# Kernel tuning notes

Hardware: AMD Instinct MI355X
Metric: run time of the kernel (lower is better)

The kernel has to match this reference:

```python
import jax, jax.numpy as jnp
import numpy as np

D_MODEL = 1024
N_HEADS = 16
HEAD_DIM = D_MODEL // N_HEADS
EPS = 1e-6


def setup_inputs() -> dict:
    key = jax.random.key(0)
    ks = jax.random.split(key, 5)
    b, s = 2, 2048
    x = jax.random.normal(ks[0], (b, s, D_MODEL), dtype=jnp.float32)
    scale = 1.0 / np.sqrt(D_MODEL)
    Wq = jax.random.normal(ks[1], (D_MODEL, D_MODEL), dtype=jnp.float32) * scale
    Wk = jax.random.normal(ks[2], (D_MODEL, D_MODEL), dtype=jnp.float32) * scale
    Wv = jax.random.normal(ks[3], (D_MODEL, D_MODEL), dtype=jnp.float32) * scale
    Wo = jax.random.normal(ks[4], (D_MODEL, D_MODEL), dtype=jnp.float32) * scale
    return {"x": x, "Wq": Wq, "Wk": Wk, "Wv": Wv, "Wo": Wo}


def _feature_map(t):
    return jax.nn.relu(t) + EPS


def reference(x, Wq, Wk, Wv, Wo):
    b, s, _ = x.shape
    # nn.Linear applies x @ W.T
    q = (x @ Wq.T).reshape(b, s, N_HEADS, HEAD_DIM)
    k = (x @ Wk.T).reshape(b, s, N_HEADS, HEAD_DIM)
    v = (x @ Wv.T).reshape(b, s, N_HEADS, HEAD_DIM)
    q = _feature_map(q).transpose(0, 2, 1, 3)  # bhsd
    k = _feature_map(k).transpose(0, 2, 1, 3)  # bhsd
    v = v.transpose(0, 2, 1, 3)                # bhsm
    # cumulative KV outer products: (b,h,s,d,m)
    kv = jnp.einsum('bhsd,bhsm->bhsdm', k, v)
    kv_cum = jnp.cumsum(kv, axis=2)
    out = jnp.einsum('bhsd,bhsdm->bhsm', q, kv_cum)
    k_cum = jnp.cumsum(k, axis=2)
    z = 1.0 / (jnp.einsum('bhsd,bhsd->bhs', q, k_cum) + EPS)
    out = out * z[..., None]
    out = out.transpose(0, 2, 1, 3).reshape(b, s, D_MODEL)
    return out @ Wo.T
```

## Files before the change

### kernel.cpp

```cpp
#include <hip/hip_runtime.h>

#define EPSF 1e-6f

typedef short bf16x8_t __attribute__((ext_vector_type(8)));
typedef float f32x4_t __attribute__((ext_vector_type(4)));

__device__ __forceinline__ ushort f2bf(float f) {
  union { float f; uint32_t u; } c; c.f = f;
  return (ushort)((c.u + 0x7FFFu + ((c.u >> 16) & 1u)) >> 16);
}
__device__ __forceinline__ float bf2f(ushort u) {
  union { uint32_t u; float f; } c; c.u = ((uint32_t)u) << 16;
  return c.f;
}

#define SWB(row, kbyte) (((row) << 7) + ((kbyte) ^ (((row) & 7) << 4)))

__global__ __launch_bounds__(256) void cvt5_kernel(
    const float4* __restrict__ x, const float4* __restrict__ wq,
    const float4* __restrict__ wk, const float4* __restrict__ wv,
    const float4* __restrict__ wo,
    ushort4* __restrict__ xb, ushort4* __restrict__ wqb,
    ushort4* __restrict__ wkb, ushort4* __restrict__ wvb,
    ushort4* __restrict__ wob)
{
  const int i = blockIdx.x * 256 + threadIdx.x;
  const float4* src; ushort4* dst; int off;
  if (i < (1 << 20)) { src = x; dst = xb; off = i; }
  else {
    const int j = i - (1 << 20);
    const int r = j >> 18;
    off = j & ((1 << 18) - 1);
    src = (r == 0) ? wq : (r == 1) ? wk : (r == 2) ? wv : wo;
    dst = (r == 0) ? wqb : (r == 1) ? wkb : (r == 2) ? wvb : wob;
  }
  const float4 v = src[off];
  ushort4 o;
  o.x = f2bf(v.x); o.y = f2bf(v.y); o.z = f2bf(v.z); o.w = f2bf(v.w);
  dst[off] = o;
}

template<int OUT_BF16, int ATOMIC>
__device__ __forceinline__ void gemm_bt_mfma(
    const ushort* __restrict__ A, const ushort* __restrict__ B,
    void* __restrict__ C, const int K,
    const int kbeg, const int kend,
    const int N, const int row0, const int col0, const bool relu)
{
  __shared__ __align__(16) uint As[2048];
  __shared__ __align__(16) uint Bs[2048];
  const int tid = threadIdx.x;
  const int lane = tid & 63;
  const int wv = tid >> 6;
  const int wr = (wv >> 1) * 64;
  const int wc = (wv & 1) * 64;

  f32x4_t acc[4][4];
#pragma unroll
  for (int m = 0; m < 4; ++m)
#pragma unroll
    for (int n = 0; n < 4; ++n) acc[m][n] = (f32x4_t){0.f, 0.f, 0.f, 0.f};

  const int fr = lane & 15;
  const int kh = (lane >> 4) * 8;

  const int chunk0 = wv * 64 + lane;
  const int chunk1 = chunk0 + 256;
  const int row_0 = chunk0 >> 2, kp0 = (chunk0 & 3) << 3;
  const int row_1 = chunk1 >> 2, kp1 = (chunk1 & 3) << 3;
  uint* ldA0 = As + (size_t)(wv * 64) * 4;
  uint* ldB0 = Bs + (size_t)(wv * 64) * 4;
  uint* ldA1 = As + (size_t)(wv * 64 + 256) * 4;
  uint* ldB1 = Bs + (size_t)(wv * 64 + 256) * 4;

  for (int k0 = kbeg; k0 < kend; k0 += 32) {
    __syncthreads();
    __builtin_amdgcn_global_load_lds(
        (const __attribute__((address_space(1))) void*)(A + (size_t)(row0 + row_0) * K + k0 + kp0),
        (__attribute__((address_space(3))) void*)ldA0, 16, 0, 0);
    __builtin_amdgcn_global_load_lds(
        (const __attribute__((address_space(1))) void*)(B + (size_t)(col0 + row_0) * K + k0 + kp0),
        (__attribute__((address_space(3))) void*)ldB0, 16, 0, 0);
    __builtin_amdgcn_global_load_lds(
        (const __attribute__((address_space(1))) void*)(A + (size_t)(row0 + row_1) * K + k0 + kp1),
        (__attribute__((address_space(3))) void*)ldA1, 16, 0, 0);
    __builtin_amdgcn_global_load_lds(
        (const __attribute__((address_space(1))) void*)(B + (size_t)(col0 + row_1) * K + k0 + kp1),
        (__attribute__((address_space(3))) void*)ldB1, 16, 0, 0);
    __syncthreads();

    bf16x8_t af[4], bfr[4];
#pragma unroll
    for (int m = 0; m < 4; ++m)
      af[m] = *(const bf16x8_t*)((const ushort*)As + (size_t)(wr + m * 16 + fr) * 32 + kh);
#pragma unroll
    for (int n = 0; n < 4; ++n)
      bfr[n] = *(const bf16x8_t*)((const ushort*)Bs + (size_t)(wc + n * 16 + fr) * 32 + kh);
#pragma unroll
    for (int m = 0; m < 4; ++m)
#pragma unroll
      for (int n = 0; n < 4; ++n)
        acc[m][n] = __builtin_amdgcn_mfma_f32_16x16x32_bf16(
            af[m], bfr[n], acc[m][n], 0, 0, 0);
  }

  const int rq = (lane >> 4) * 4;
#pragma unroll
  for (int m = 0; m < 4; ++m) {
#pragma unroll
    for (int r = 0; r < 4; ++r) {
      const size_t grow = (size_t)(row0 + wr + m * 16 + rq + r);
#pragma unroll
      for (int n = 0; n < 4; ++n) {
        float val = acc[m][n][r];
        if (relu) val = fmaxf(val, 0.f) + EPSF;
        const size_t gcol = (size_t)(col0 + wc + n * 16 + fr);
        if (ATOMIC)        atomicAdd(&((float*)C)[grow * N + gcol], val);
        else if (OUT_BF16) ((ushort*)C)[grow * N + gcol] = f2bf(val);
        else               ((float*)C)[grow * N + gcol] = val;
      }
    }
  }
}

__global__ __launch_bounds__(256) void qkv_gemm_kernel(
    const ushort* __restrict__ xb,
    const ushort* __restrict__ wqb, const ushort* __restrict__ wkb,
    const ushort* __restrict__ wvb,
    ushort* __restrict__ q, ushort* __restrict__ k, ushort* __restrict__ v)
{
  const int which = blockIdx.y >> 3;
  const int bcol = blockIdx.y & 7;
  const ushort* B = (which == 0) ? wqb : (which == 1) ? wkb : wvb;
  ushort* C = (which == 0) ? q : (which == 1) ? k : v;
  gemm_bt_mfma<1, 0>(xb, B, C, 1024, 0, 1024, 1024,
                     blockIdx.x * 128, bcol * 128, which < 2);
}

__global__ __launch_bounds__(256) void out_gemm_kernel(
    const ushort* __restrict__ at, const ushort* __restrict__ wob,
    float* __restrict__ out)
{
  const int kb0 = blockIdx.z * 512;
  gemm_bt_mfma<0, 1>(at, wob, out, 1024, kb0, kb0 + 512, 1024,
                     blockIdx.x * 128, blockIdx.y * 128, false);
}


__global__ __launch_bounds__(256) void chunk_sums_kernel(
    const ushort* __restrict__ kbuf, const ushort* __restrict__ vbuf,
    float* __restrict__ kvsum, float* __restrict__ ksum)
{
  __shared__ __align__(16) uint Kt[2048];
  __shared__ __align__(16) uint Vt[2048];
  const int chunk = blockIdx.x;
  const int seq = blockIdx.y;
  const int b = seq >> 4, h = seq & 15;
  const int tid = threadIdx.x;
  const size_t base = ((size_t)b * 2048 + chunk * 64) * 1024 + h * 64;

#pragma unroll
  for (int r = 0; r < 2; ++r) {
    const int idx = tid + (r << 8);
    const int j = idx >> 3;
    const int e0 = (idx & 7) << 3;
    const bf16x8_t kv8 = *(const bf16x8_t*)(kbuf + base + (size_t)j * 1024 + e0);
    const bf16x8_t vv8 = *(const bf16x8_t*)(vbuf + base + (size_t)j * 1024 + e0);
#pragma unroll
    for (int t = 0; t < 8; ++t) {
      *(ushort*)((char*)Kt + SWB(e0 + t, j * 2)) = (ushort)kv8[t];
      *(ushort*)((char*)Vt + SWB(e0 + t, j * 2)) = (ushort)vv8[t];
    }
  }
  __syncthreads();

  if (tid < 64) {
    float s = 0.f;
#pragma unroll
    for (int g = 0; g < 8; ++g) {
      const bf16x8_t kr = *(const bf16x8_t*)((char*)Kt + SWB(tid, g * 16));
#pragma unroll
      for (int t = 0; t < 8; ++t) s += bf2f((ushort)kr[t]);
    }
    ksum[((size_t)seq * 32 + chunk) * 64 + tid] = s;
  }

  const int lane = tid & 63;
  const int wv = tid >> 6;
  const int wm = (wv >> 1) * 32;
  const int wd = (wv & 1) * 32;
  const int fr = lane & 15;
  const int khb = (lane >> 4) * 16;

  f32x4_t acc[2][2];
#pragma unroll
  for (int m = 0; m < 2; ++m)
#pragma unroll
    for (int n = 0; n < 2; ++n) acc[m][n] = (f32x4_t){0.f, 0.f, 0.f, 0.f};

#pragma unroll
  for (int kk = 0; kk < 2; ++kk) {
    bf16x8_t av[2], bk[2];
#pragma unroll
    for (int m = 0; m < 2; ++m)
      av[m] = *(const bf16x8_t*)((char*)Vt + SWB(wm + m * 16 + fr, kk * 64 + khb));
#pragma unroll
    for (int n = 0; n < 2; ++n)
      bk[n] = *(const bf16x8_t*)((char*)Kt + SWB(wd + n * 16 + fr, kk * 64 + khb));
#pragma unroll
    for (int m = 0; m < 2; ++m)
#pragma unroll
      for (int n = 0; n < 2; ++n)
        acc[m][n] = __builtin_amdgcn_mfma_f32_16x16x32_bf16(
            av[m], bk[n], acc[m][n], 0, 0, 0);
  }

  const size_t kvbase = ((size_t)seq * 32 + chunk) << 12;
  const int rq = (lane >> 4) * 4;
#pragma unroll
  for (int m = 0; m < 2; ++m)
#pragma unroll
    for (int r = 0; r < 4; ++r) {
      const int mrow = wm + m * 16 + rq + r;
#pragma unroll
      for (int n = 0; n < 2; ++n) {
        const int dcol = wd + n * 16 + fr;
        kvsum[kvbase + (size_t)mrow * 64 + dcol] = acc[m][n][r];
      }
    }
}

__global__ __launch_bounds__(256) void scan_kernel(
    float* __restrict__ kvsum, float* __restrict__ ksum)
{
  const int slice = blockIdx.x & 15;
  const int seq = blockIdx.x >> 4;
  const int e = slice * 256 + threadIdx.x;
  const size_t base = ((size_t)seq << 17) + e;
  float vals[32];
#pragma unroll
  for (int c = 0; c < 32; ++c) vals[c] = kvsum[base + ((size_t)c << 12)];
  float run = 0.f;
#pragma unroll
  for (int c = 0; c < 32; ++c) {
    const float t = vals[c];
    kvsum[base + ((size_t)c << 12)] = run;
    run += t;
  }
  if (slice == 0 && threadIdx.x < 64) {
    const size_t kb = (size_t)seq * 2048 + threadIdx.x;
    float kv2[32];
#pragma unroll
    for (int c = 0; c < 32; ++c) kv2[c] = ksum[kb + (size_t)c * 64];
    float run2 = 0.f;
#pragma unroll
    for (int c = 0; c < 32; ++c) {
      const float t = kv2[c];
      ksum[kb + (size_t)c * 64] = run2;
      run2 += t;
    }
  }
}

__global__ __launch_bounds__(256) void attn_chunk_kernel(
    const ushort* __restrict__ qbuf, const ushort* __restrict__ kbuf,
    const ushort* __restrict__ vbuf, const float* __restrict__ kvsum,
    const float* __restrict__ ksum, ushort* __restrict__ attn)
{
  __shared__ __align__(16) uint Qs[2048];
  __shared__ __align__(16) uint Ks[2048];
  __shared__ __align__(16) uint Vt[2048];
  __shared__ __align__(16) uint Pl[2048];
  __shared__ float ksp[64];
  __shared__ float zinv[64];
  const int chunk = blockIdx.x;
  const int seq = blockIdx.y;
  const int b = seq >> 4, h = seq & 15;
  const int tid = threadIdx.x;
  const size_t base = ((size_t)b * 2048 + chunk * 64) * 1024 + h * 64;

#pragma unroll
  for (int r = 0; r < 2; ++r) {
    const int idx = tid + (r << 8);
    const int row = idx >> 3;
    const int e0 = (idx & 7) << 3;
    const int kb = e0 << 1;
    *(bf16x8_t*)((char*)Qs + SWB(row, kb)) =
        *(const bf16x8_t*)(qbuf + base + (size_t)row * 1024 + e0);
    *(bf16x8_t*)((char*)Ks + SWB(row, kb)) =
        *(const bf16x8_t*)(kbuf + base + (size_t)row * 1024 + e0);
    const bf16x8_t vv8 = *(const bf16x8_t*)(vbuf + base + (size_t)row * 1024 + e0);
#pragma unroll
    for (int t = 0; t < 8; ++t)
      *(ushort*)((char*)Vt + SWB(e0 + t, row * 2)) = (ushort)vv8[t];
  }
  if (tid < 64) ksp[tid] = ksum[((size_t)seq * 32 + chunk) * 64 + tid];
  __syncthreads();

  const int lane = tid & 63;
  const int wv = tid >> 6;
  const int wr = (wv >> 1) * 32;
  const int wc = (wv & 1) * 32;
  const int fr = lane & 15;
  const int khb = (lane >> 4) * 16;
  const int rq = (lane >> 4) * 4;

  f32x4_t sf[2][2];
#pragma unroll
  for (int m = 0; m < 2; ++m)
#pragma unroll
    for (int n = 0; n < 2; ++n) sf[m][n] = (f32x4_t){0.f, 0.f, 0.f, 0.f};
#pragma unroll
  for (int kk = 0; kk < 2; ++kk) {
    bf16x8_t aq[2], bk[2];
#pragma unroll
    for (int m = 0; m < 2; ++m)
      aq[m] = *(const bf16x8_t*)((char*)Qs + SWB(wr + m * 16 + fr, kk * 64 + khb));
#pragma unroll
    for (int n = 0; n < 2; ++n)
      bk[n] = *(const bf16x8_t*)((char*)Ks + SWB(wc + n * 16 + fr, kk * 64 + khb));
#pragma unroll
    for (int m = 0; m < 2; ++m)
#pragma unroll
      for (int n = 0; n < 2; ++n)
        sf[m][n] = __builtin_amdgcn_mfma_f32_16x16x32_bf16(
            aq[m], bk[n], sf[m][n], 0, 0, 0);
  }
  __syncthreads();

#pragma unroll
  for (int m = 0; m < 2; ++m)
#pragma unroll
    for (int r = 0; r < 4; ++r) {
      const int i = wr + m * 16 + rq + r;
#pragma unroll
      for (int n = 0; n < 2; ++n) {
        const int j = wc + n * 16 + fr;
        const float pv = (j <= i) ? sf[m][n][r] : 0.f;
        *(ushort*)((char*)Pl + SWB(i, j * 2)) = f2bf(pv);
      }
    }
  const size_t kvbase = ((size_t)seq * 32 + chunk) << 12;
#pragma unroll
  for (int r = 0; r < 2; ++r) {
    const int idx = tid + (r << 8);
    const int mrow = idx >> 3;
    const int d0 = (idx & 7) << 3;
    const float4 lo = *(const float4*)(kvsum + kvbase + (size_t)mrow * 64 + d0);
    const float4 hi = *(const float4*)(kvsum + kvbase + (size_t)mrow * 64 + d0 + 4);
    bf16x8_t kv8;
    kv8[0] = (short)f2bf(lo.x); kv8[1] = (short)f2bf(lo.y);
    kv8[2] = (short)f2bf(lo.z); kv8[3] = (short)f2bf(lo.w);
    kv8[4] = (short)f2bf(hi.x); kv8[5] = (short)f2bf(hi.y);
    kv8[6] = (short)f2bf(hi.z); kv8[7] = (short)f2bf(hi.w);
    *(bf16x8_t*)((char*)Ks + SWB(mrow, d0 << 1)) = kv8;
  }
  __syncthreads();

  if (tid < 64) {
    const int i = tid;
    float dsum = 0.f, ssum = 0.f;
#pragma unroll
    for (int g = 0; g < 8; ++g) {
      const bf16x8_t qr = *(const bf16x8_t*)((char*)Qs + SWB(i, g * 16));
      const bf16x8_t pr = *(const bf16x8_t*)((char*)Pl + SWB(i, g * 16));
#pragma unroll
      for (int t = 0; t < 8; ++t) {
        dsum = fmaf(bf2f((ushort)qr[t]), ksp[g * 8 + t], dsum);
        ssum += bf2f((ushort)pr[t]);
      }
    }
    zinv[i] = 1.f / (dsum + ssum + EPSF);
  }

  f32x4_t of[2][2];
#pragma unroll
  for (int m = 0; m < 2; ++m)
#pragma unroll
    for (int n = 0; n < 2; ++n) of[m][n] = (f32x4_t){0.f, 0.f, 0.f, 0.f};
#pragma unroll
  for (int kk = 0; kk < 2; ++kk) {
    bf16x8_t ap[2], bv[2];
#pragma unroll
    for (int m = 0; m < 2; ++m)
      ap[m] = *(const bf16x8_t*)((char*)Pl + SWB(wr + m * 16 + fr, kk * 64 + khb));
#pragma unroll
    for (int n = 0; n < 2; ++n)
      bv[n] = *(const bf16x8_t*)((char*)Vt + SWB(wc + n * 16 + fr, kk * 64 + khb));
#pragma unroll
    for (int m = 0; m < 2; ++m)
#pragma unroll
      for (int n = 0; n < 2; ++n)
        of[m][n] = __builtin_amdgcn_mfma_f32_16x16x32_bf16(
            ap[m], bv[n], of[m][n], 0, 0, 0);
  }
#pragma unroll
  for (int kk = 0; kk < 2; ++kk) {
    bf16x8_t aq[2], bkv[2];
#pragma unroll
    for (int m = 0; m < 2; ++m)
      aq[m] = *(const bf16x8_t*)((char*)Qs + SWB(wr + m * 16 + fr, kk * 64 + khb));
#pragma unroll
    for (int n = 0; n < 2; ++n)
      bkv[n] = *(const bf16x8_t*)((char*)Ks + SWB(wc + n * 16 + fr, kk * 64 + khb));
#pragma unroll
    for (int m = 0; m < 2; ++m)
#pragma unroll
      for (int n = 0; n < 2; ++n)
        of[m][n] = __builtin_amdgcn_mfma_f32_16x16x32_bf16(
            aq[m], bkv[n], of[m][n], 0, 0, 0);
  }
  __syncthreads();

#pragma unroll
  for (int m = 0; m < 2; ++m)
#pragma unroll
    for (int r = 0; r < 4; ++r) {
      const int i = wr + m * 16 + rq + r;
      const float z = zinv[i];
#pragma unroll
      for (int n = 0; n < 2; ++n) {
        const int mcol = wc + n * 16 + fr;
        attn[base + (size_t)i * 1024 + mcol] = f2bf(of[m][n][r] * z);
      }
    }
}

extern "C" void kernel_launch(void* const* d_in, const int* in_sizes, int n_in,
                              void* d_out, int out_size, void* d_ws, size_t ws_size,
                              hipStream_t stream)
{
  (void)in_sizes; (void)n_in; (void)ws_size;
  const float* x  = (const float*)d_in[0];
  const float* Wq = (const float*)d_in[1];
  const float* Wk = (const float*)d_in[2];
  const float* Wv = (const float*)d_in[3];
  const float* Wo = (const float*)d_in[4];
  float* out = (float*)d_out;

  const size_t NM = (size_t)4096 * 1024;
  ushort* xb  = (ushort*)d_ws;
  ushort* wqb = xb + NM;
  ushort* wkb = wqb + (1 << 20);
  ushort* wvb = wkb + (1 << 20);
  ushort* wob = wvb + (1 << 20);
  ushort* qb  = wob + (1 << 20);
  ushort* kb  = qb + NM;
  ushort* vb  = kb + NM;
  ushort* at  = vb + NM;
  float*  ksm = (float*)(at + NM);
  float*  kvs = ksm + 65536;

  hipMemsetAsync(d_out, 0, (size_t)out_size * sizeof(float), stream);

  cvt5_kernel<<<8192, 256, 0, stream>>>(
      (const float4*)x, (const float4*)Wq, (const float4*)Wk,
      (const float4*)Wv, (const float4*)Wo,
      (ushort4*)xb, (ushort4*)wqb, (ushort4*)wkb, (ushort4*)wvb, (ushort4*)wob);
  qkv_gemm_kernel<<<dim3(32, 24), 256, 0, stream>>>(xb, wqb, wkb, wvb, qb, kb, vb);
  chunk_sums_kernel<<<dim3(32, 32), 256, 0, stream>>>(kb, vb, kvs, ksm);
  scan_kernel<<<512, 256, 0, stream>>>(kvs, ksm);
  attn_chunk_kernel<<<dim3(32, 32), 256, 0, stream>>>(qb, kb, vb, kvs, ksm, at);
  out_gemm_kernel<<<dim3(32, 8, 2), 256, 0, stream>>>(at, wob, out);
}
```

Baseline: 183.2 us.

## Fuse x fp32-to-bf16 conversion into QKV GEMM, drop split-K atomics and memset

The separate conversion of x to bf16 is removed: the QKV GEMM now loads fp32 x directly and packs it to bf16 in registers before writing to LDS. The output GEMM no longer splits K across two blocks with atomic adds, so the memset of the output and the atomic traffic go away, though the grid halves. The scan now writes the prefix KV sums as bf16, so the attention kernel reads half the bytes and skips its conversion. The costs are synchronous register loads in place of async global-to-LDS copies for A, and less parallelism in the output GEMM.

After: 167.4 us. 8.7% less time.

```diff
diff --git a/kernel.cpp b/kernel.cpp
--- a/kernel.cpp
+++ b/kernel.cpp
@@ -16,35 +16,27 @@
 
 #define SWB(row, kbyte) (((row) << 7) + ((kbyte) ^ (((row) & 7) << 4)))
 
-__global__ __launch_bounds__(256) void cvt5_kernel(
-    const float4* __restrict__ x, const float4* __restrict__ wq,
-    const float4* __restrict__ wk, const float4* __restrict__ wv,
-    const float4* __restrict__ wo,
-    ushort4* __restrict__ xb, ushort4* __restrict__ wqb,
-    ushort4* __restrict__ wkb, ushort4* __restrict__ wvb,
-    ushort4* __restrict__ wob)
+__global__ __launch_bounds__(256) void cvtw_kernel(
+    const float4* __restrict__ wq, const float4* __restrict__ wk,
+    const float4* __restrict__ wv, const float4* __restrict__ wo,
+    ushort4* __restrict__ wqb, ushort4* __restrict__ wkb,
+    ushort4* __restrict__ wvb, ushort4* __restrict__ wob)
 {
   const int i = blockIdx.x * 256 + threadIdx.x;
-  const float4* src; ushort4* dst; int off;
-  if (i < (1 << 20)) { src = x; dst = xb; off = i; }
-  else {
-    const int j = i - (1 << 20);
-    const int r = j >> 18;
-    off = j & ((1 << 18) - 1);
-    src = (r == 0) ? wq : (r == 1) ? wk : (r == 2) ? wv : wo;
-    dst = (r == 0) ? wqb : (r == 1) ? wkb : (r == 2) ? wvb : wob;
-  }
+  const int r = i >> 18;
+  const int off = i & ((1 << 18) - 1);
+  const float4* src = (r == 0) ? wq : (r == 1) ? wk : (r == 2) ? wv : wo;
+  ushort4* dst = (r == 0) ? wqb : (r == 1) ? wkb : (r == 2) ? wvb : wob;
   const float4 v = src[off];
   ushort4 o;
   o.x = f2bf(v.x); o.y = f2bf(v.y); o.z = f2bf(v.z); o.w = f2bf(v.w);
   dst[off] = o;
 }
 
-template<int OUT_BF16, int ATOMIC>
+template<int OUT_BF16, int A_FP32>
 __device__ __forceinline__ void gemm_bt_mfma(
-    const ushort* __restrict__ A, const ushort* __restrict__ B,
+    const void* __restrict__ Av, const ushort* __restrict__ B,
     void* __restrict__ C, const int K,
-    const int kbeg, const int kend,
     const int N, const int row0, const int col0, const bool relu)
 {
   __shared__ __align__(16) uint As[2048];
@@ -73,18 +65,38 @@
   uint* ldA1 = As + (size_t)(wv * 64 + 256) * 4;
   uint* ldB1 = Bs + (size_t)(wv * 64 + 256) * 4;
 
-  for (int k0 = kbeg; k0 < kend; k0 += 32) {
+  for (int k0 = 0; k0 < K; k0 += 32) {
     __syncthreads();
-    __builtin_amdgcn_global_load_lds(
-        (const __attribute__((address_space(1))) void*)(A + (size_t)(row0 + row_0) * K + k0 + kp0),
-        (__attribute__((address_space(3))) void*)ldA0, 16, 0, 0);
+    if (A_FP32) {
+      const float* Af = (const float*)Av;
+#pragma unroll
+      for (int is = 0; is < 2; ++is) {
+        const int s = tid + (is << 8);
+        const int row = s >> 2, kq = (s & 3) << 3;
+        const float* src = Af + (size_t)(row0 + row) * K + k0 + kq;
+        const float4 f0 = *(const float4*)(src);
+        const float4 f1 = *(const float4*)(src + 4);
+        uint p0, p1, p2, p3;
+        asm("v_cvt_pk_bf16_f32 %0, %1, %2" : "=v"(p0) : "v"(f0.x), "v"(f0.y));
+        asm("v_cvt_pk_bf16_f32 %0, %1, %2" : "=v"(p1) : "v"(f0.z), "v"(f0.w));
+        asm("v_cvt_pk_bf16_f32 %0, %1, %2" : "=v"(p2) : "v"(f1.x), "v"(f1.y));
+        asm("v_cvt_pk_bf16_f32 %0, %1, %2" : "=v"(p3) : "v"(f1.z), "v"(f1.w));
+        uint4 pk; pk.x = p0; pk.y = p1; pk.z = p2; pk.w = p3;
+        *(uint4*)(As + (size_t)s * 4) = pk;
+      }
+    } else {
+      const ushort* Ab = (const ushort*)Av;
+      __builtin_amdgcn_global_load_lds(
+          (const __attribute__((address_space(1))) void*)(Ab + (size_t)(row0 + row_0) * K + k0 + kp0),
+          (__attribute__((address_space(3))) void*)ldA0, 16, 0, 0);
+      __builtin_amdgcn_global_load_lds(
+          (const __attribute__((address_space(1))) void*)(Ab + (size_t)(row0 + row_1) * K + k0 + kp1),
+          (__attribute__((address_space(3))) void*)ldA1, 16, 0, 0);
+    }
     __builtin_amdgcn_global_load_lds(
         (const __attribute__((address_space(1))) void*)(B + (size_t)(col0 + row_0) * K + k0 + kp0),
         (__attribute__((address_space(3))) void*)ldB0, 16, 0, 0);
     __builtin_amdgcn_global_load_lds(
-        (const __attribute__((address_space(1))) void*)(A + (size_t)(row0 + row_1) * K + k0 + kp1),
-        (__attribute__((address_space(3))) void*)ldA1, 16, 0, 0);
-    __builtin_amdgcn_global_load_lds(
         (const __attribute__((address_space(1))) void*)(B + (size_t)(col0 + row_1) * K + k0 + kp1),
         (__attribute__((address_space(3))) void*)ldB1, 16, 0, 0);
     __syncthreads();
@@ -115,16 +127,15 @@
         float val = acc[m][n][r];
         if (relu) val = fmaxf(val, 0.f) + EPSF;
         const size_t gcol = (size_t)(col0 + wc + n * 16 + fr);
-        if (ATOMIC)        atomicAdd(&((float*)C)[grow * N + gcol], val);
-        else if (OUT_BF16) ((ushort*)C)[grow * N + gcol] = f2bf(val);
-        else               ((float*)C)[grow * N + gcol] = val;
+        if (OUT_BF16) ((ushort*)C)[grow * N + gcol] = f2bf(val);
+        else          ((float*)C)[grow * N + gcol] = val;
       }
     }
   }
 }
 
 __global__ __launch_bounds__(256) void qkv_gemm_kernel(
-    const ushort* __restrict__ xb,
+    const float* __restrict__ x,
     const ushort* __restrict__ wqb, const ushort* __restrict__ wkb,
     const ushort* __restrict__ wvb,
     ushort* __restrict__ q, ushort* __restrict__ k, ushort* __restrict__ v)
@@ -133,7 +144,7 @@
   const int bcol = blockIdx.y & 7;
   const ushort* B = (which == 0) ? wqb : (which == 1) ? wkb : wvb;
   ushort* C = (which == 0) ? q : (which == 1) ? k : v;
-  gemm_bt_mfma<1, 0>(xb, B, C, 1024, 0, 1024, 1024,
+  gemm_bt_mfma<1, 1>(x, B, C, 1024, 1024,
                      blockIdx.x * 128, bcol * 128, which < 2);
 }
 
@@ -141,8 +152,7 @@
     const ushort* __restrict__ at, const ushort* __restrict__ wob,
     float* __restrict__ out)
 {
-  const int kb0 = blockIdx.z * 512;
-  gemm_bt_mfma<0, 1>(at, wob, out, 1024, kb0, kb0 + 512, 1024,
+  gemm_bt_mfma<0, 0>(at, wob, out, 1024, 1024,
                      blockIdx.x * 128, blockIdx.y * 128, false);
 }
 
@@ -231,7 +241,8 @@
 }
 
 __global__ __launch_bounds__(256) void scan_kernel(
-    float* __restrict__ kvsum, float* __restrict__ ksum)
+    const float* __restrict__ kvsum, ushort* __restrict__ kvsb,
+    float* __restrict__ ksum)
 {
   const int slice = blockIdx.x & 15;
   const int seq = blockIdx.x >> 4;
@@ -243,9 +254,8 @@
   float run = 0.f;
 #pragma unroll
   for (int c = 0; c < 32; ++c) {
-    const float t = vals[c];
-    kvsum[base + ((size_t)c << 12)] = run;
-    run += t;
+    kvsb[base + ((size_t)c << 12)] = f2bf(run);
+    run += vals[c];
   }
   if (slice == 0 && threadIdx.x < 64) {
     const size_t kb = (size_t)seq * 2048 + threadIdx.x;
@@ -264,7 +274,7 @@
 
 __global__ __launch_bounds__(256) void attn_chunk_kernel(
     const ushort* __restrict__ qbuf, const ushort* __restrict__ kbuf,
-    const ushort* __restrict__ vbuf, const float* __restrict__ kvsum,
+    const ushort* __restrict__ vbuf, const ushort* __restrict__ kvsb,
     const float* __restrict__ ksum, ushort* __restrict__ attn)
 {
   __shared__ __align__(16) uint Qs[2048];
@@ -346,13 +356,7 @@
     const int idx = tid + (r << 8);
     const int mrow = idx >> 3;
     const int d0 = (idx & 7) << 3;
-    const float4 lo = *(const float4*)(kvsum + kvbase + (size_t)mrow * 64 + d0);
-    const float4 hi = *(const float4*)(kvsum + kvbase + (size_t)mrow * 64 + d0 + 4);
-    bf16x8_t kv8;
-    kv8[0] = (short)f2bf(lo.x); kv8[1] = (short)f2bf(lo.y);
-    kv8[2] = (short)f2bf(lo.z); kv8[3] = (short)f2bf(lo.w);
-    kv8[4] = (short)f2bf(hi.x); kv8[5] = (short)f2bf(hi.y);
-    kv8[6] = (short)f2bf(hi.z); kv8[7] = (short)f2bf(hi.w);
+    const bf16x8_t kv8 = *(const bf16x8_t*)(kvsb + kvbase + (size_t)mrow * 64 + d0);
     *(bf16x8_t*)((char*)Ks + SWB(mrow, d0 << 1)) = kv8;
   }
   __syncthreads();
@@ -430,7 +434,7 @@
                               void* d_out, int out_size, void* d_ws, size_t ws_size,
                               hipStream_t stream)
 {
-  (void)in_sizes; (void)n_in; (void)ws_size;
+  (void)in_sizes; (void)n_in; (void)out_size; (void)ws_size;
   const float* x  = (const float*)d_in[0];
   const float* Wq = (const float*)d_in[1];
   const float* Wk = (const float*)d_in[2];
@@ -439,8 +443,7 @@
   float* out = (float*)d_out;
 
   const size_t NM = (size_t)4096 * 1024;
-  ushort* xb  = (ushort*)d_ws;
-  ushort* wqb = xb + NM;
+  ushort* wqb = (ushort*)d_ws;
   ushort* wkb = wqb + (1 << 20);
   ushort* wvb = wkb + (1 << 20);
   ushort* wob = wvb + (1 << 20);
@@ -450,16 +453,14 @@
   ushort* at  = vb + NM;
   float*  ksm = (float*)(at + NM);
   float*  kvs = ksm + 65536;
-
-  hipMemsetAsync(d_out, 0, (size_t)out_size * sizeof(float), stream);
-
-  cvt5_kernel<<<8192, 256, 0, stream>>>(
-      (const float4*)x, (const float4*)Wq, (const float4*)Wk,
-      (const float4*)Wv, (const float4*)Wo,
-      (ushort4*)xb, (ushort4*)wqb, (ushort4*)wkb, (ushort4*)wvb, (ushort4*)wob);
-  qkv_gemm_kernel<<<dim3(32, 24), 256, 0, stream>>>(xb, wqb, wkb, wvb, qb, kb, vb);
+  ushort* kvsb = (ushort*)(kvs + NM);
+
+  cvtw_kernel<<<4096, 256, 0, stream>>>(
+      (const float4*)Wq, (const float4*)Wk, (const float4*)Wv, (const float4*)Wo,
+      (ushort4*)wqb, (ushort4*)wkb, (ushort4*)wvb, (ushort4*)wob);
+  qkv_gemm_kernel<<<dim3(32, 24), 256, 0, stream>>>(x, wqb, wkb, wvb, qb, kb, vb);
   chunk_sums_kernel<<<dim3(32, 32), 256, 0, stream>>>(kb, vb, kvs, ksm);
-  scan_kernel<<<512, 256, 0, stream>>>(kvs, ksm);
-  attn_chunk_kernel<<<dim3(32, 32), 256, 0, stream>>>(qb, kb, vb, kvs, ksm, at);
-  out_gemm_kernel<<<dim3(32, 8, 2), 256, 0, stream>>>(at, wob, out);
-}
+  scan_kernel<<<512, 256, 0, stream>>>(kvs, kvsb, ksm);
+  attn_chunk_kernel<<<dim3(32, 32), 256, 0, stream>>>(qb, kb, vb, kvsb, ksm, at);
+  out_gemm_kernel<<<dim3(32, 8), 256, 0, stream>>>(at, wob, out);
+}
```
